# Kernel optimization log

Hardware: AMD Instinct MI355X
Metric: run time of the kernel (lower is better)

The kernel has to match this reference:

```python
import jax, jax.numpy as jnp
import numpy as np

N_HIDDEN = 49  # number of Linear(64,64)+ReLU layers between the input and output projections
D_IN, D_HID, D_OUT = 10, 64, 10
BATCH = 1048576


def setup_inputs() -> dict:
    key = jax.random.key(0)
    ks = jax.random.split(key, 7)
    s_in = 1.0 / np.sqrt(D_IN)
    s_hid = 1.0 / np.sqrt(D_HID)
    return {
        "x": jax.random.normal(ks[0], (BATCH, D_IN), dtype=jnp.float32),
        # torch nn.Linear stores weight as [out_features, in_features]
        "w_in": jax.random.uniform(ks[1], (D_HID, D_IN), jnp.float32, -s_in, s_in),
        "b_in": jax.random.uniform(ks[2], (D_HID,), jnp.float32, -s_in, s_in),
        "w_hid": jax.random.uniform(ks[3], (N_HIDDEN, D_HID, D_HID), jnp.float32, -s_hid, s_hid),
        "b_hid": jax.random.uniform(ks[4], (N_HIDDEN, D_HID), jnp.float32, -s_hid, s_hid),
        "w_out": jax.random.uniform(ks[5], (D_OUT, D_HID), jnp.float32, -s_hid, s_hid),
        "b_out": jax.random.uniform(ks[6], (D_OUT,), jnp.float32, -s_hid, s_hid),
    }


def reference(x, w_in, b_in, w_hid, b_hid, w_out, b_out):
    # Flatten (no-op for 2D), then Linear(10,64)+ReLU
    h = jax.nn.relu(x @ w_in.T + b_in)  # [B, 64]

    def step(h, wb):
        w, b = wb
        return jax.nn.relu(h @ w.T + b), None

    h, _ = jax.lax.scan(step, h, (w_hid, b_hid))
    return h @ w_out.T + b_out  # final Linear(64,10), no activation
```

## Files before the change

### kernel.cpp

```cpp
#include <hip/hip_runtime.h>
#include <stdint.h>

typedef _Float16 half8 __attribute__((ext_vector_type(8)));
typedef float f32x16 __attribute__((ext_vector_type(16)));
typedef float f32x4  __attribute__((ext_vector_type(4)));

#define NH 49

__device__ __forceinline__ uint32_t pk2(float a, float b){
  auto p = __builtin_amdgcn_cvt_pkrtz(a, b);
  return __builtin_bit_cast(uint32_t, p);
}
__device__ __forceinline__ uint32_t relu2(uint32_t p){
  uint32_t r, z = 0u;
  asm("v_pk_max_f16 %0, %1, %2" : "=v"(r) : "v"(p), "v"(z));
  return r;
}

template<int RH>
__device__ __forceinline__ void cvt4(const f32x16& c, uint32_t* d){
  d[0] = relu2(pk2(c[8*RH+0], c[8*RH+1]));
  d[1] = relu2(pk2(c[8*RH+2], c[8*RH+3]));
  d[2] = relu2(pk2(c[8*RH+4], c[8*RH+5]));
  d[3] = relu2(pk2(c[8*RH+6], c[8*RH+7]));
}

__device__ __forceinline__ half8 toh8(const uint32_t* d){
  union { uint32_t u[4]; half8 h; } v;
  v.u[0]=d[0]; v.u[1]=d[1]; v.u[2]=d[2]; v.u[3]=d[3];
  return v.h;
}

__device__ __forceinline__ f32x16 bias_c(const float* sbase, int mt, int hi){
  f32x16 c;
  const float* b = sbase + 32*mt + 4*hi;
  #pragma unroll
  for (int g=0; g<4; ++g){
    f32x4 v = *(const f32x4*)(b + 8*g);
    c[4*g+0]=v[0]; c[4*g+1]=v[1]; c[4*g+2]=v[2]; c[4*g+3]=v[3];
  }
  return c;
}

__device__ __forceinline__ int phi(int k){
  return (k & 51) | ((k & 4) << 1) | ((k & 8) >> 1);
}

__global__ void prep_weights(const float* __restrict__ w_in,
                             const float* __restrict__ w_hid,
                             const float* __restrict__ w_out,
                             half8* __restrict__ wf)
{
  int bid = blockIdx.x;
  int lane = threadIdx.x;
  int hi = lane >> 5, lo = lane & 31;
  half8 f;
  if (bid < 2){
    int mt = bid, row = 32*mt + lo;
    #pragma unroll
    for (int e=0; e<8; ++e){
      int k = 8*hi + e;
      f[e] = (k < 10) ? (_Float16)w_in[row*10 + k] : (_Float16)0.f;
    }
  } else if (bid < 394){
    int t = bid - 2;
    int l = t >> 3, kt = (t >> 1) & 3, mt = t & 1;
    int row = 32*mt + lo;
    #pragma unroll
    for (int e=0; e<8; ++e){
      int k = 16*kt + 8*hi + e;
      f[e] = (_Float16)w_hid[(l*64 + row)*64 + phi(k)];
    }
  } else {
    int kt = bid - 394;
    #pragma unroll
    for (int e=0; e<8; ++e){
      int k = 16*kt + 8*hi + e;
      f[e] = (lo < 10) ? (_Float16)w_out[lo*64 + phi(k)] : (_Float16)0.f;
    }
  }
  wf[bid*64 + lane] = f;
}

__device__ __forceinline__ f32x16 mfma16(half8 a, half8 b, f32x16 c){
  return __builtin_amdgcn_mfma_f32_32x32x16_f16(a, b, c, 0, 0, 0);
}

__global__ __launch_bounds__(256, 2) void mlp_fused(
    const float* __restrict__ x,
    const float* __restrict__ b_in,
    const float* __restrict__ b_hid,
    const float* __restrict__ b_out,
    const half8* __restrict__ wfrag,
    float* __restrict__ out)
{
  __shared__ __attribute__((aligned(16))) float sb[50*64 + 32];
  for (int i = threadIdx.x; i < 64; i += 256)     sb[i]      = b_in[i];
  for (int i = threadIdx.x; i < NH*64; i += 256)  sb[64 + i] = b_hid[i];
  if (threadIdx.x < 32) sb[3200 + threadIdx.x] = (threadIdx.x < 10) ? b_out[threadIdx.x] : 0.f;
  __syncthreads();

  const int lane = threadIdx.x & 63;
  const int wid  = threadIdx.x >> 6;
  const int hi   = lane >> 5;
  const int col  = lane & 31;
  const long rowbase = ((long)blockIdx.x * 4 + wid) * 128;
  const half8* whid = wfrag + 128;
  const float* sbh  = sb + 64;

  f32x16 acc[4][2];

  {
    half8 a0 = wfrag[lane];
    half8 a1 = wfrag[64 + lane];
    f32x16 cb0 = bias_c(sb, 0, hi);
    f32x16 cb1 = bias_c(sb, 1, hi);
    #pragma unroll
    for (int bt=0; bt<4; ++bt){
      const float* xr = x + (rowbase + bt*32 + col) * 10;
      float xv[8];
      if (hi == 0){
        #pragma unroll
        for (int j=0;j<8;++j) xv[j] = xr[j];
      } else {
        xv[0]=xr[8]; xv[1]=xr[9];
        #pragma unroll
        for (int j=2;j<8;++j) xv[j]=0.f;
      }
      uint32_t d[4] = { pk2(xv[0],xv[1]), pk2(xv[2],xv[3]),
                        pk2(xv[4],xv[5]), pk2(xv[6],xv[7]) };
      half8 bx = toh8(d);
      acc[bt][0] = mfma16(a0, bx, cb0);
      acc[bt][1] = mfma16(a1, bx, cb1);
    }
  }

  #pragma unroll 1
  for (int h = 0; h < NH; ++h){
    const half8* wl = whid + h*512;
    half8 w[8];
    #pragma unroll
    for (int f=0; f<8; ++f) w[f] = wl[f*64 + lane];
    const float* bl = sbh + (h << 6);
    f32x16 cb0 = bias_c(bl, 0, hi);
    f32x16 cb1 = bias_c(bl, 1, hi);

    #pragma unroll
    for (int bt=0; bt<4; ++bt){
      uint32_t bfr[16];
      cvt4<0>(acc[bt][0], bfr + 0);
      cvt4<1>(acc[bt][0], bfr + 4);
      cvt4<0>(acc[bt][1], bfr + 8);
      cvt4<1>(acc[bt][1], bfr + 12);
      __builtin_amdgcn_s_setprio(1);
      #pragma unroll
      for (int kt=0; kt<4; ++kt){
        half8 bb = toh8(bfr + 4*kt);
        acc[bt][0] = mfma16(w[2*kt    ], bb, kt ? acc[bt][0] : cb0);
        acc[bt][1] = mfma16(w[2*kt + 1], bb, kt ? acc[bt][1] : cb1);
      }
      __builtin_amdgcn_s_setprio(0);
    }
  }

  const half8* wo = wfrag + 128 + 392*64;
  f32x16 cbo = bias_c(sb + 3200, 0, hi);
  f32x16 oacc[4];
  #pragma unroll
  for (int bt=0; bt<4; ++bt){
    uint32_t bfr[16];
    cvt4<0>(acc[bt][0], bfr + 0);
    cvt4<1>(acc[bt][0], bfr + 4);
    cvt4<0>(acc[bt][1], bfr + 8);
    cvt4<1>(acc[bt][1], bfr + 12);
    #pragma unroll
    for (int kt=0; kt<4; ++kt){
      half8 aw = wo[kt*64 + lane];
      half8 bb = toh8(bfr + 4*kt);
      oacc[bt] = (kt==0) ? mfma16(aw, bb, cbo) : mfma16(aw, bb, oacc[bt]);
    }
  }
  #pragma unroll
  for (int bt=0; bt<4; ++bt){
    float* orow = out + (rowbase + bt*32 + col) * 10;
    if (hi == 0){
      *(float2*)(orow + 0) = make_float2(oacc[bt][0], oacc[bt][1]);
      *(float2*)(orow + 2) = make_float2(oacc[bt][2], oacc[bt][3]);
      *(float2*)(orow + 8) = make_float2(oacc[bt][4], oacc[bt][5]);
    } else {
      *(float2*)(orow + 4) = make_float2(oacc[bt][0], oacc[bt][1]);
      *(float2*)(orow + 6) = make_float2(oacc[bt][2], oacc[bt][3]);
    }
  }
}

extern "C" void kernel_launch(void* const* d_in, const int* in_sizes, int n_in,
                              void* d_out, int out_size, void* d_ws, size_t ws_size,
                              hipStream_t stream)
{
  const float* x     = (const float*)d_in[0];
  const float* w_in  = (const float*)d_in[1];
  const float* b_in  = (const float*)d_in[2];
  const float* w_hid = (const float*)d_in[3];
  const float* b_hid = (const float*)d_in[4];
  const float* w_out = (const float*)d_in[5];
  const float* b_out = (const float*)d_in[6];
  half8* wf = (half8*)d_ws;

  prep_weights<<<398, 64, 0, stream>>>(w_in, w_hid, w_out, wf);
  mlp_fused<<<2048, 256, 0, stream>>>(x, b_in, b_hid, b_out, wf, (float*)d_out);
}
```

Baseline: 311.3 us.

## Prefetch next layer's weight fragments and software-pipeline conversion with MFMA

Restructures the hidden-layer loop into a two-layer unrolled body. Half of the next layer's weight fragments are prefetched into double-buffered registers while the current layer computes. The fp16 pack/relu conversion of the next batch tile is interleaved ahead of the MFMAs of the current tile, so VALU work overlaps matrix ops. The aim is to hide global weight-load latency and conversion latency behind MFMA, at the cost of more live registers, which could cause spills at 2 blocks per CU.

```diff
diff --git a/kernel.cpp b/kernel.cpp
--- a/kernel.cpp
+++ b/kernel.cpp
@@ -24,6 +24,9 @@
   d[2] = relu2(pk2(c[8*RH+4], c[8*RH+5]));
   d[3] = relu2(pk2(c[8*RH+6], c[8*RH+7]));
 }
+__device__ __forceinline__ void cvt16(const f32x16& a0, const f32x16& a1, uint32_t* d){
+  cvt4<0>(a0, d+0); cvt4<1>(a0, d+4); cvt4<0>(a1, d+8); cvt4<1>(a1, d+12);
+}
 
 __device__ __forceinline__ half8 toh8(const uint32_t* d){
   union { uint32_t u[4]; half8 h; } v;
@@ -84,6 +87,48 @@
 
 __device__ __forceinline__ f32x16 mfma16(half8 a, half8 b, f32x16 c){
   return __builtin_amdgcn_mfma_f32_32x32x16_f16(a, b, c, 0, 0, 0);
+}
+
+__device__ __forceinline__ void mfma8x(f32x16& am0, f32x16& am1,
+    const half8 (&wlo)[4], const half8 (&whi)[4],
+    const uint32_t* bfr, const f32x16& cb0, const f32x16& cb1)
+{
+  __builtin_amdgcn_s_setprio(1);
+  half8 b0 = toh8(bfr+0);
+  am0 = mfma16(wlo[0], b0, cb0);  am1 = mfma16(wlo[1], b0, cb1);
+  half8 b1 = toh8(bfr+4);
+  am0 = mfma16(wlo[2], b1, am0);  am1 = mfma16(wlo[3], b1, am1);
+  half8 b2 = toh8(bfr+8);
+  am0 = mfma16(whi[0], b2, am0);  am1 = mfma16(whi[1], b2, am1);
+  half8 b3 = toh8(bfr+12);
+  am0 = mfma16(whi[2], b3, am0);  am1 = mfma16(whi[3], b3, am1);
+  __builtin_amdgcn_s_setprio(0);
+}
+
+__device__ __forceinline__ void layer_body(
+    const half8* frags_this, const half8* frags_next,
+    half8 (&wlo)[4], half8 (&wnext)[4],
+    const float* bl, int lane, int hi,
+    f32x16 (&acc)[4][2], bool pref)
+{
+  half8 whi_[4];
+  #pragma unroll
+  for (int f=0; f<4; ++f) whi_[f] = frags_this[(4+f)*64 + lane];
+  f32x16 cb0 = bias_c(bl, 0, hi);
+  f32x16 cb1 = bias_c(bl, 1, hi);
+  uint32_t bfrA[16], bfrB[16];
+  cvt16(acc[0][0], acc[0][1], bfrA);
+  cvt16(acc[1][0], acc[1][1], bfrB);
+  mfma8x(acc[0][0], acc[0][1], wlo, whi_, bfrA, cb0, cb1);
+  cvt16(acc[2][0], acc[2][1], bfrA);
+  mfma8x(acc[1][0], acc[1][1], wlo, whi_, bfrB, cb0, cb1);
+  if (pref){
+    #pragma unroll
+    for (int f=0; f<4; ++f) wnext[f] = frags_next[f*64 + lane];
+  }
+  cvt16(acc[3][0], acc[3][1], bfrB);
+  mfma8x(acc[2][0], acc[2][1], wlo, whi_, bfrA, cb0, cb1);
+  mfma8x(acc[3][0], acc[3][1], wlo, whi_, bfrB, cb0, cb1);
 }
 
 __global__ __launch_bounds__(256, 2) void mlp_fused(
@@ -109,6 +154,10 @@
   const float* sbh  = sb + 64;
 
   f32x16 acc[4][2];
+
+  half8 wA[4], wB[4];
+  #pragma unroll
+  for (int f=0; f<4; ++f) wA[f] = whid[f*64 + lane];
 
   {
     half8 a0 = wfrag[lane];
@@ -136,32 +185,14 @@
   }
 
   #pragma unroll 1
-  for (int h = 0; h < NH; ++h){
-    const half8* wl = whid + h*512;
-    half8 w[8];
-    #pragma unroll
-    for (int f=0; f<8; ++f) w[f] = wl[f*64 + lane];
-    const float* bl = sbh + (h << 6);
-    f32x16 cb0 = bias_c(bl, 0, hi);
-    f32x16 cb1 = bias_c(bl, 1, hi);
-
-    #pragma unroll
-    for (int bt=0; bt<4; ++bt){
-      uint32_t bfr[16];
-      cvt4<0>(acc[bt][0], bfr + 0);
-      cvt4<1>(acc[bt][0], bfr + 4);
-      cvt4<0>(acc[bt][1], bfr + 8);
-      cvt4<1>(acc[bt][1], bfr + 12);
-      __builtin_amdgcn_s_setprio(1);
-      #pragma unroll
-      for (int kt=0; kt<4; ++kt){
-        half8 bb = toh8(bfr + 4*kt);
-        acc[bt][0] = mfma16(w[2*kt    ], bb, kt ? acc[bt][0] : cb0);
-        acc[bt][1] = mfma16(w[2*kt + 1], bb, kt ? acc[bt][1] : cb1);
-      }
-      __builtin_amdgcn_s_setprio(0);
-    }
-  }
+  for (int h = 0; h < NH-1; h += 2){
+    layer_body(whid + h*512,     whid + (h+1)*512, wA, wB,
+               sbh + (h<<6),     lane, hi, acc, true);
+    layer_body(whid + (h+1)*512, whid + (h+2)*512, wB, wA,
+               sbh + ((h+1)<<6), lane, hi, acc, (h+2) < NH);
+  }
+  layer_body(whid + (NH-1)*512, whid, wA, wB,
+             sbh + ((NH-1)<<6), lane, hi, acc, false);
 
   const half8* wo = wfrag + 128 + 392*64;
   f32x16 cbo = bias_c(sb + 3200, 0, hi);
@@ -169,10 +200,7 @@
   #pragma unroll
   for (int bt=0; bt<4; ++bt){
     uint32_t bfr[16];
-    cvt4<0>(acc[bt][0], bfr + 0);
-    cvt4<1>(acc[bt][0], bfr + 4);
-    cvt4<0>(acc[bt][1], bfr + 8);
-    cvt4<1>(acc[bt][1], bfr + 12);
+    cvt16(acc[bt][0], acc[bt][1], bfr);
     #pragma unroll
     for (int kt=0; kt<4; ++kt){
       half8 aw = wo[kt*64 + lane];
```

Result: no change. 315.4 us (+1.3%).
